# Optimization experiments

Measured on AMD Instinct MI355X. Metric: run time of the kernel, lower is better.

## Reference

```python
import jax, jax.numpy as jnp
import numpy as np
import math

B, S, E, H = 2, 1024, 1024, 8
HD = E // H
M, W, K, GH, R, MR = 128, 32, 8, 128, 8, 8
ATTN_ALPHA, GATE_TEMP, CONTENT_MIX = 3.0, 1.0, 0.25
FFN_H = 4 * E


def _layernorm(z, g, b):
    mu = jnp.mean(z, axis=-1, keepdims=True)
    var = jnp.var(z, axis=-1, keepdims=True)
    return (z - mu) * jax.lax.rsqrt(var + 1e-5) * g + b


def _topk_sparse(logits, k, temp):
    # faithful to torch topk_sparse_weights: hard + (soft - hard).detach()
    soft = jax.nn.softmax(logits / max(temp, 1e-6), axis=-1)
    idx = jax.lax.top_k(soft, k)[1]
    hard = jax.nn.one_hot(idx, logits.shape[-1], dtype=soft.dtype).sum(axis=-2)
    hard = hard / (hard.sum(axis=-1, keepdims=True) + 1e-8)
    return hard + jax.lax.stop_gradient(soft - hard)


def _pos_and_window():
    rel = jnp.arange(-(S - 1), S, dtype=jnp.float32)  # [2S-1]
    p1 = rel / S
    p2 = jnp.sign(rel) * jnp.sqrt(jnp.abs(rel) + 1e-6) / math.sqrt(S)
    pos_kern = jnp.stack([p1, p2], axis=-1)  # [2S-1, 2]
    d = jnp.arange(S, dtype=jnp.float32)
    sigma = S / 4.0
    win = jnp.exp(-(d ** 2) / (2.0 * sigma ** 2))  # [S]
    return pos_kern, win


def setup_inputs() -> dict:
    key = jax.random.key(0)
    ks = jax.random.split(key, 20)
    rn = lambda i, shape, s: jax.random.normal(ks[i], shape, dtype=jnp.float32) * s
    scale = 1.0 / math.sqrt(HD)
    return {
        'x': rn(0, (B, S, E), 1.0),
        'v_w': rn(1, (E, E), 0.02), 'v_b': jnp.zeros((E,), jnp.float32),
        'out_w': rn(2, (E, E), 0.02), 'out_b': jnp.zeros((E,), jnp.float32),
        'qmod_w': rn(3, (E, H), 0.02), 'qmod_b': jnp.zeros((H,), jnp.float32),
        'kmod_w': rn(4, (E, H), 0.02), 'kmod_b': jnp.zeros((H,), jnp.float32),
        'gate_w1': rn(5, (H, E, GH), 0.02), 'gate_b1': jnp.zeros((H, GH), jnp.float32),
        'gate_w2': rn(6, (H, GH, M), 0.02), 'gate_b2': jnp.zeros((H, M), jnp.float32),
        'mod_w1': rn(7, (H, E, GH), 0.02), 'mod_b1': jnp.zeros((H, GH), jnp.float32),
        'mod_w2': rn(8, (H, GH, MR), 0.02), 'mod_b2': jnp.zeros((H, MR), jnp.float32),
        'mod_basis': rn(9, (H, MR, M), 0.05),
        'freqs': rn(10, (H, M, W, 2), 1.5),
        'amps': rn(11, (H, M, W), 0.02) + 0.5,
        'phases': rn(12, (H, M, W), math.pi),
        'content_wq': rn(13, (H, HD, R), scale),
        'content_wk': rn(14, (H, HD, R), scale),
        'ffn_w1': rn(15, (E, FFN_H), 0.02), 'ffn_b1': jnp.zeros((FFN_H,), jnp.float32),
        'ffn_w2': rn(16, (FFN_H, E), 0.02), 'ffn_b2': jnp.zeros((E,), jnp.float32),
        'ln_attn_g': jnp.ones((E,), jnp.float32), 'ln_attn_b': jnp.zeros((E,), jnp.float32),
        'ln_ffn_g': jnp.ones((E,), jnp.float32), 'ln_ffn_b': jnp.zeros((E,), jnp.float32),
    }


def reference(x, v_w, v_b, out_w, out_b, qmod_w, qmod_b, kmod_w, kmod_b,
              gate_w1, gate_b1, gate_w2, gate_b2, mod_w1, mod_b1, mod_w2, mod_b2,
              mod_basis, freqs, amps, phases, content_wq, content_wk,
              ffn_w1, ffn_b1, ffn_w2, ffn_b2, ln_attn_g, ln_attn_b, ln_ffn_g, ln_ffn_b):
    pos_kern, win = _pos_and_window()
    # --- per-sequence gating over mask library (top-k sparse routing) ---
    pooled = x.mean(axis=1)  # [B,E]
    gh = jax.nn.relu(jnp.einsum('be,heg->bhg', pooled, gate_w1) + gate_b1)
    glog = jnp.einsum('bhg,hgm->bhm', gh, gate_w2) + gate_b2  # [B,H,M]
    wsel = _topk_sparse(glog, K, GATE_TEMP)
    mh = jax.nn.relu(jnp.einsum('be,heg->bhg', pooled, mod_w1) + mod_b1)
    mr = jnp.einsum('bhg,hgr->bhr', mh, mod_w2) + mod_b2  # [B,H,MR]
    mod = jnp.einsum('bhr,hrm->bhm', mr, mod_basis)
    wmod = wsel * (1.0 + mod)  # [B,H,M]
    # --- wave-interference synthesis of relative-position kernels ---
    dots = jnp.einsum('ld,hmwd->hmwl', pos_kern, freqs)  # [H,M,W,2S-1]
    waves = jnp.sin(2.0 * math.pi * dots + phases[..., None]) * amps[..., None]
    kernels = waves.sum(axis=2)  # [H,M,2S-1]
    kern = jnp.einsum('bhm,hml->bhl', wmod, kernels)  # [B,H,2S-1]
    # --- Toeplitz gather into causal score matrix ---
    i = jnp.arange(S)
    rel_idx = (i[None, :] - i[:, None]) + (S - 1)  # index of rel = j - i
    scores = kern[:, :, rel_idx]  # [B,H,S,S]
    dist = jnp.clip(i[:, None] - i[None, :], 0, S - 1)
    scores = scores * win[dist]
    qs = x @ qmod_w + qmod_b  # [B,S,H]
    km = x @ kmod_w + kmod_b
    logits = ATTN_ALPHA * scores + qs.transpose(0, 2, 1)[..., None] + km.transpose(0, 2, 1)[:, :, None, :]
    # --- low-rank content term ---
    xh = x.reshape(B, S, H, HD)
    qc = jnp.einsum('bshd,hdr->bhsr', xh, content_wq)
    kc = jnp.einsum('bshd,hdr->bhsr', xh, content_wk)
    logits = logits + CONTENT_MIX * jnp.einsum('bhsr,bhtr->bhst', qc, kc)
    causal = i[:, None] >= i[None, :]
    logits = jnp.where(causal, logits, -jnp.inf)
    attn = jax.nn.softmax(logits, axis=-1)
    v = (x @ v_w + v_b).reshape(B, S, H, HD)
    o = jnp.einsum('bhst,bthd->bshd', attn, v).reshape(B, S, E)
    o = o @ out_w + out_b
    y = _layernorm(x + o, ln_attn_g, ln_attn_b)
    f = jax.nn.gelu(y @ ffn_w1 + ffn_b1) @ ffn_w2 + ffn_b2
    return _layernorm(y + f, ln_ffn_g, ln_ffn_b)
```

## Files before the change

kernel.cpp:

```cpp
#include <hip/hip_runtime.h>
#include <math.h>
#include <stdint.h>

namespace {

constexpr int B_ = 2, S_ = 1024, E_ = 1024, H_ = 8, HD_ = 128;
constexpr int M_ = 128, W_ = 32, GH_ = 128, R_ = 8, MR_ = 8, FFNH_ = 4096;
constexpr int SCH = 32;
constexpr int SPC = S_ / SCH;

typedef __bf16 bf16;
typedef _Float16 f16;
typedef __attribute__((ext_vector_type(8))) __bf16 bf16x8;
typedef __attribute__((ext_vector_type(4))) __bf16 bf16x4;
typedef __attribute__((ext_vector_type(4))) _Float16 f16x4;
typedef __attribute__((ext_vector_type(4))) float f32x4;

__device__ inline float gelu_tanh(float u) {
  float u3 = u * u * u;
  return 0.5f * u * (1.f + tanhf(0.7978845608028654f * (u + 0.044715f * u3)));
}

__device__ __forceinline__ void gl_lds16(const void* g, void* l) {
  __builtin_amdgcn_global_load_lds((const __attribute__((address_space(1))) void*)g,
                                   (__attribute__((address_space(3))) void*)l, 16, 0, 0);
}

template <int NB>
__device__ __forceinline__ void gemm_body(
    const bf16* __restrict__ A, const bf16* __restrict__ BT,
    f16* __restrict__ P, int N, int K, int Kslice, size_t strideB, size_t mn,
    int lin, int gx, int gy, bf16* Asb, bf16* Bsb) {
  int t = threadIdx.x;
  int by = lin % gy;
  int rem = lin / gy;
  int bx = rem % gx;
  int z = rem / gx;
  int bb = z % NB;
  int k0 = (z / NB) * Kslice;
  const bf16* Bbase = BT + (size_t)bb * strideB;
  int row0 = by * 128, col0 = bx * 128;
  int lane = t & 63, wid = t >> 6;
  int wr = wid >> 1, wc = wid & 1;

  const bf16* AgP[4];
  const bf16* BgP[4];
  int ldo[4];
#pragma unroll
  for (int j = 0; j < 4; ++j) {
    int p = t + j * 256;
    int sub = p >> 9;
    int pp = p & 511;
    int rt = ((pp >> 6) << 4) | (pp & 15);
    int kb = (pp >> 4) & 3;
    AgP[j] = A + (size_t)(row0 + rt) * K + k0 + sub * 32 + kb * 8;
    BgP[j] = Bbase + (size_t)(col0 + rt) * K + k0 + sub * 32 + kb * 8;
    ldo[j] = sub * 4096 + pp * 8;
  }

  f32x4 acc[4][4];
#pragma unroll
  for (int m = 0; m < 4; ++m)
#pragma unroll
    for (int n = 0; n < 4; ++n) acc[m][n] = (f32x4){0.f, 0.f, 0.f, 0.f};

#pragma unroll
  for (int j = 0; j < 4; ++j) {
    gl_lds16(AgP[j], &Asb[ldo[j]]);
    gl_lds16(BgP[j], &Bsb[ldo[j]]);
  }

  const int nt = Kslice >> 6;
  for (int kt = 0; kt < nt; ++kt) {
    int cur = kt & 1;
    __syncthreads();
    if (kt + 1 < nt) {
      size_t go = (size_t)(kt + 1) * 64;
      int nb = cur ^ 1;
#pragma unroll
      for (int j = 0; j < 4; ++j) {
        gl_lds16(AgP[j] + go, &Asb[nb * 8192 + ldo[j]]);
        gl_lds16(BgP[j] + go, &Bsb[nb * 8192 + ldo[j]]);
      }
    }
#pragma unroll
    for (int kk = 0; kk < 2; ++kk) {
      bf16x8 af[4], bfr[4];
#pragma unroll
      for (int m = 0; m < 4; ++m)
        af[m] = *(const bf16x8*)&Asb[cur * 8192 + kk * 4096 + ((wr * 4 + m) * 64 + lane) * 8];
#pragma unroll
      for (int n = 0; n < 4; ++n)
        bfr[n] = *(const bf16x8*)&Bsb[cur * 8192 + kk * 4096 + ((wc * 4 + n) * 64 + lane) * 8];
#pragma unroll
      for (int m = 0; m < 4; ++m)
#pragma unroll
        for (int n = 0; n < 4; ++n)
          acc[m][n] = __builtin_amdgcn_mfma_f32_16x16x32_bf16(af[m], bfr[n], acc[m][n], 0, 0, 0);
    }
  }

  f16* Pz = P + (size_t)z * mn;
  int r0 = row0 + wr * 64, c0 = col0 + wc * 64;
#pragma unroll
  for (int m = 0; m < 4; ++m)
#pragma unroll
    for (int n = 0; n < 4; ++n) {
      int col = c0 + n * 16 + (lane & 15);
#pragma unroll
      for (int reg = 0; reg < 4; ++reg) {
        int row = r0 + m * 16 + ((lane >> 4) << 2) + reg;
        Pz[(size_t)row * N + col] = (f16)acc[m][n][reg];
      }
    }
}

__global__ __launch_bounds__(256) void k_prep(
    const float* __restrict__ x, bf16* __restrict__ xb,
    const float* __restrict__ v_w, bf16* __restrict__ vwT,
    const float* __restrict__ out_w, bf16* __restrict__ outwT,
    const float* __restrict__ ffn_w1, bf16* __restrict__ ffn1T,
    const float* __restrict__ ffn_w2, bf16* __restrict__ ffn2T,
    const float* __restrict__ qmw, const float* __restrict__ kmw,
    const float* __restrict__ cwq, const float* __restrict__ cwk,
    bf16* __restrict__ wcat, float* __restrict__ part,
    const float* __restrict__ freqs, const float* __restrict__ amps,
    const float* __restrict__ phases, float* __restrict__ kerns) {
  __shared__ float tile[32][33];
  __shared__ float f0[W_], f1[W_], am[W_], ph[W_];
  int b = blockIdx.x, t = threadIdx.x;
  if (b < 2048) {
    size_t i = ((size_t)b * 256 + t) * 4;
    float4 v = *(const float4*)(x + i);
    bf16x4 o;
    o.x = (bf16)v.x; o.y = (bf16)v.y; o.z = (bf16)v.z; o.w = (bf16)v.w;
    *(bf16x4*)(xb + i) = o;
    return;
  }
  if (b < 12288) {
    const float* w; bf16* wT; int K, N, bx, by;
    if (b < 3072) {
      w = v_w; wT = vwT; K = 1024; N = 1024;
      int l = b - 2048; bx = l & 31; by = l >> 5;
    } else if (b < 4096) {
      w = out_w; wT = outwT; K = 1024; N = 1024;
      int l = b - 3072; bx = l & 31; by = l >> 5;
    } else if (b < 8192) {
      w = ffn_w1; wT = ffn1T; K = 1024; N = 4096;
      int l = b - 4096; bx = l & 127; by = l >> 7;
    } else {
      w = ffn_w2; wT = ffn2T; K = 4096; N = 1024;
      int l = b - 8192; bx = l & 31; by = l >> 5;
    }
    int n0 = bx * 32, k0 = by * 32;
    int tx = t & 31, ty = t >> 5;
    for (int r = ty; r < 32; r += 8) tile[r][tx] = w[(size_t)(k0 + r) * N + n0 + tx];
    __syncthreads();
    for (int r = ty; r < 32; r += 8) wT[(size_t)(n0 + r) * K + k0 + tx] = (bf16)tile[tx][r];
    return;
  }
  if (b < 13312) {
    int idx = (b - 12288) * 256 + t;
    int n = idx >> 10, k = idx & 1023;
    float v = 0.f;
    if (n < 8) {
      v = qmw[k * 8 + n];
    } else if (n < 16) {
      v = kmw[k * 8 + (n - 8)];
    } else if (n < 80) {
      int u = n - 16, h = u >> 3, r = u & 7;
      int kk = k - h * 128;
      if (kk >= 0 && kk < 128) v = cwq[((size_t)h * 128 + kk) * 8 + r];
    } else if (n < 144) {
      int u = n - 80, h = u >> 3, r = u & 7;
      int kk = k - h * 128;
      if (kk >= 0 && kk < 128) v = cwk[((size_t)h * 128 + kk) * 8 + r];
    }
    wcat[idx] = (bf16)v;
    return;
  }
  if (b < 13376) {
    int b0 = b - 13312;
    int bb = b0 / SCH, c = b0 % SCH;
    const float* xp = x + (size_t)bb * S_ * E_ + (size_t)c * SPC * E_;
    float acc[4] = {0.f, 0.f, 0.f, 0.f};
    for (int s = 0; s < SPC; ++s) {
      const float* row = xp + (size_t)s * E_;
#pragma unroll
      for (int q = 0; q < 4; ++q) acc[q] += row[t + q * 256];
    }
    float* pp = part + (size_t)b0 * E_;
#pragma unroll
    for (int q = 0; q < 4; ++q) pp[t + q * 256] = acc[q];
    return;
  }
  {
    int blk = b - 13376;
    int lt = blk & 3;
    int hm = blk >> 2;
    if (t < W_) {
      f0[t] = freqs[((size_t)hm * W_ + t) * 2 + 0];
      f1[t] = freqs[((size_t)hm * W_ + t) * 2 + 1];
      am[t] = amps[(size_t)hm * W_ + t];
      ph[t] = phases[(size_t)hm * W_ + t];
    }
    __syncthreads();
    int l = lt * 256 + t;
    float rel = (float)(l - (S_ - 1));
    float p1 = rel * (1.0f / S_);
    float p2 = (rel < 0.f) ? (-sqrtf(-rel + 1e-6f) * (1.0f / 32.0f)) : 0.f;
    const float TWO_PI = 6.28318530717958647692f;
    float acc = 0.f;
#pragma unroll
    for (int w = 0; w < W_; ++w)
      acc += am[w] * __sinf(TWO_PI * (f0[w] * p1 + f1[w] * p2) + ph[w]);
    kerns[(size_t)hm * S_ + l] = acc;
  }
}

__global__ __launch_bounds__(256) void k_qkg(
    const bf16* __restrict__ xb, const bf16* __restrict__ wcatT,
    f16* __restrict__ P,
    const float* __restrict__ part,
    const float* __restrict__ gw1, const float* __restrict__ mw1,
    float2* __restrict__ gpart) {
  __shared__ bf16 Asb[2 * 8192];
  __shared__ bf16 Bsb[2 * 8192];
  __shared__ float spool[2][64];
  __shared__ float red[2][2][128];
  int b = blockIdx.x, t = threadIdx.x;
  if (b < 256) {
    int lin = (b & 7) * 32 + (b >> 3);
    gemm_body<1>(xb, wcatT, P, 256, E_, 128, 0, (size_t)2048 * 256,
                 lin, 2, 16, Asb, Bsb);
    return;
  }
  int b0 = b - 256;
  int chunk = b0 & 15, h = (b0 >> 4) & 7, mat = b0 >> 7;
  const float* w = mat ? mw1 : gw1;
  if (t < 128) {
    int bb = t >> 6;
    int e = chunk * 64 + (t & 63);
    float s = 0.f;
    for (int c = 0; c < SCH; ++c) s += part[(size_t)(bb * SCH + c) * E_ + e];
    spool[bb][t & 63] = s * (1.0f / S_);
  }
  __syncthreads();
  int g = t & 127, half = t >> 7;
  int e0 = chunk * 64 + half * 32;
  const float* wp = w + (size_t)h * E_ * GH_ + (size_t)e0 * GH_ + g;
  float a0 = 0.f, a1 = 0.f;
#pragma unroll 8
  for (int r = 0; r < 32; ++r) {
    float wv = wp[(size_t)r * GH_];
    a0 += spool[0][half * 32 + r] * wv;
    a1 += spool[1][half * 32 + r] * wv;
  }
  red[half][0][g] = a0;
  red[half][1][g] = a1;
  __syncthreads();
  if (half == 0) {
    float2 o;
    o.x = red[0][0][g] + red[1][0][g];
    o.y = red[0][1][g] + red[1][1][g];
    gpart[(((size_t)mat * H_ + h) * 16 + chunk) * 128 + g] = o;
  }
}

__global__ __launch_bounds__(256) void k_fg2(
    const f16* __restrict__ P, const float* __restrict__ qmb,
    const float* __restrict__ kmb, float* __restrict__ qsT,
    float* __restrict__ kmT, float* __restrict__ qc, float* __restrict__ kc,
    const float2* __restrict__ gpart,
    const float* __restrict__ gb1, const float* __restrict__ gw2, const float* __restrict__ gb2,
    const float* __restrict__ mb1, const float* __restrict__ mw2, const float* __restrict__ mb2,
    const float* __restrict__ mbasis, float* __restrict__ wmod) {
  __shared__ float ghs[GH_], mhs[GH_], glog[M_], mrs[MR_];
  __shared__ float red2[2][128];
  __shared__ float rbuf[128];
  int blk = blockIdx.x, t = threadIdx.x;
  if (blk < 2048) {
    if (t >= 144) return;
    int row = blk;
    int b = row >> 10, s = row & 1023;
    const size_t mn = (size_t)2048 * 256;
    float sum = 0.f;
#pragma unroll
    for (int z = 0; z < 8; ++z) sum += (float)P[(size_t)z * mn + (size_t)row * 256 + t];
    if (t < 8) {
      qsT[((size_t)(b * 8 + t)) * 1024 + s] = sum + qmb[t];
    } else if (t < 16) {
      kmT[((size_t)(b * 8 + t - 8)) * 1024 + s] = sum + kmb[t - 8];
    } else if (t < 80) {
      int u = t - 16, h = u >> 3, r = u & 7;
      qc[(((size_t)(b * 8 + h)) * 1024 + s) * 8 + r] = sum;
    } else {
      int u = t - 80, h = u >> 3, r = u & 7;
      kc[(((size_t)(b * 8 + h)) * 1024 + s) * 8 + r] = sum;
    }
    return;
  }
  int bh = blk - 2048;
  int b = bh >> 3, h = bh & 7;
  {
    int g = t & 127, mat = t >> 7;
    const float2* pp = gpart + ((size_t)mat * H_ + h) * 16 * 128 + g;
    float acc = 0.f;
#pragma unroll
    for (int c = 0; c < 16; ++c) {
      float2 v = pp[(size_t)c * 128];
      acc += b ? v.y : v.x;
    }
    acc += (mat ? mb1 : gb1)[h * GH_ + g];
    acc = fmaxf(acc, 0.f);
    if (mat == 0) ghs[g] = acc; else mhs[g] = acc;
  }
  __syncthreads();
  {
    int m = t & 127, half = t >> 7;
    float acc = 0.f;
    const float* wp = gw2 + (size_t)h * GH_ * M_ + m;
#pragma unroll 4
    for (int g = half * 64; g < half * 64 + 64; ++g)
      acc += ghs[g] * wp[(size_t)g * M_];
    red2[half][m] = acc;
  }
  __syncthreads();
  if (t < 128) glog[t] = red2[0][t] + red2[1][t] + gb2[h * M_ + t];
  if (t < 64) {
    int r = t & 7, seg = t >> 3;
    float acc = 0.f;
    const float* wp = mw2 + (size_t)h * GH_ * MR_ + r;
    for (int g = seg * 16; g < seg * 16 + 16; ++g) acc += mhs[g] * wp[(size_t)g * MR_];
    acc += __shfl_xor(acc, 8);
    acc += __shfl_xor(acc, 16);
    acc += __shfl_xor(acc, 32);
    if (t < 8) mrs[t] = acc + mb2[h * MR_ + t];
  }
  __syncthreads();
  if (t < 128) rbuf[t] = glog[t];
  __syncthreads();
  for (int off = 64; off >= 1; off >>= 1) {
    if (t < off) rbuf[t] = fmaxf(rbuf[t], rbuf[t + off]);
    __syncthreads();
  }
  float mx = rbuf[0];
  __syncthreads();
  float ev = 0.f;
  if (t < 128) ev = expf(glog[t] - mx);
  __syncthreads();
  if (t < 128) rbuf[t] = ev;
  __syncthreads();
  for (int off = 64; off >= 1; off >>= 1) {
    if (t < off) rbuf[t] += rbuf[t + off];
    __syncthreads();
  }
  float inv = 1.f / rbuf[0];
  if (t < 128) {
    float wsel = ev * inv;
    float md = 0.f;
#pragma unroll
    for (int r = 0; r < MR_; ++r) md += mrs[r] * mbasis[((size_t)h * MR_ + r) * M_ + t];
    wmod[bh * M_ + t] = wsel * (1.f + md);
  }
}

__global__ __launch_bounds__(256) void k_cv(
    const float* __restrict__ qc, const float* __restrict__ kc,
    bf16* __restrict__ cont,
    const float* __restrict__ wmod, const float* __restrict__ kerns,
    float* __restrict__ swin,
    const bf16* __restrict__ vwT, const bf16* __restrict__ xb,
    f16* __restrict__ P) {
  __shared__ bf16 Asb[2 * 8192];
  __shared__ bf16 Bsb[2 * 8192];
  __shared__ float wm[M_];
  int b = blockIdx.x, t = threadIdx.x;
  if (b >= 1088) {
    int l = b - 1088;
    int lin = (l & 7) * 64 + (l >> 3);
    gemm_body<2>(vwT, xb, P, S_, E_, 256, (size_t)S_ * E_, (size_t)1024 * 1024,
                 lin, 8, 8, Asb, Bsb);
    return;
  }
  int jt = b & 7, it = (b >> 3) & 7, bh = b >> 6;
  if (bh == 16) {
    int blk = it * 8 + jt;
    int dt = blk & 3;
    int sbh = blk >> 2;
    int h = sbh & 7;
    if (t < M_) wm[t] = wmod[sbh * M_ + t];
    __syncthreads();
    int d = dt * 256 + t;
    int l = (S_ - 1) - d;
    float acc = 0.f;
    for (int m = 0; m < M_; ++m) acc += wm[m] * kerns[((size_t)h * M_ + m) * S_ + l];
    float dd = (float)d;
    float win = expf(-dd * dd * (1.0f / 131072.0f));
    swin[(size_t)sbh * S_ + d] = 3.0f * win * acc;
    return;
  }
  if (jt > it) return;
  int w = t >> 6, lane = t & 63;
  int ln = lane & 15, ko = lane >> 4;
  int i0 = it * 128 + w * 32;
  int j0 = jt * 128;

  bf16x8 av[2];
#pragma unroll
  for (int mi = 0; mi < 2; ++mi) {
    bf16x8 a;
#pragma unroll
    for (int k = 0; k < 8; ++k) a[k] = (bf16)0.f;
    if (ko == 0) {
      const float* qp = &qc[((size_t)bh * S_ + i0 + mi * 16 + ln) * 8];
      float4 q0 = *(const float4*)qp;
      float4 q1 = *(const float4*)(qp + 4);
      a[0] = (bf16)q0.x; a[1] = (bf16)q0.y; a[2] = (bf16)q0.z; a[3] = (bf16)q0.w;
      a[4] = (bf16)q1.x; a[5] = (bf16)q1.y; a[6] = (bf16)q1.z; a[7] = (bf16)q1.w;
    }
    av[mi] = a;
  }
  bf16x8 bv[8];
#pragma unroll
  for (int nb = 0; nb < 8; ++nb) {
    bf16x8 bb;
#pragma unroll
    for (int k = 0; k < 8; ++k) bb[k] = (bf16)0.f;
    if (ko == 0) {
      const float* kp = &kc[((size_t)bh * S_ + j0 + nb * 16 + ln) * 8];
      float4 k0 = *(const float4*)kp;
      float4 k1 = *(const float4*)(kp + 4);
      bb[0] = (bf16)k0.x; bb[1] = (bf16)k0.y; bb[2] = (bf16)k0.z; bb[3] = (bf16)k0.w;
      bb[4] = (bf16)k1.x; bb[5] = (bf16)k1.y; bb[6] = (bf16)k1.z; bb[7] = (bf16)k1.w;
    }
    bv[nb] = bb;
  }
  f32x4 acc[2][8];
#pragma unroll
  for (int mi = 0; mi < 2; ++mi)
#pragma unroll
    for (int nb = 0; nb < 8; ++nb) {
      acc[mi][nb] = (f32x4){0.f, 0.f, 0.f, 0.f};
      acc[mi][nb] = __builtin_amdgcn_mfma_f32_16x16x32_bf16(av[mi], bv[nb], acc[mi][nb], 0, 0, 0);
    }
  bf16* cb = cont + ((size_t)bh << 20);
#pragma unroll
  for (int mi = 0; mi < 2; ++mi)
#pragma unroll
    for (int nb = 0; nb < 8; ++nb) {
      int col = j0 + nb * 16 + ln;
#pragma unroll
      for (int reg = 0; reg < 4; ++reg) {
        int row = i0 + mi * 16 + ko * 4 + reg;
        cb[(size_t)row * S_ + col] = (bf16)acc[mi][nb][reg];
      }
    }
}

template <bool GELU, bool RES, bool OUTF32, bool OUTBF16>
__global__ __launch_bounds__(256) void k_gemm_mfma(
    const bf16* __restrict__ A, const bf16* __restrict__ BT,
    const float* __restrict__ bias, const float* __restrict__ res,
    float* __restrict__ C, bf16* __restrict__ Cb, int N, int K) {
  __shared__ bf16 Asb[2][8192];
  __shared__ bf16 Bsb[2][8192];
  int t = threadIdx.x;
  int gx = gridDim.x, gy = gridDim.y;
  int nwg = gx * gy;
  int lin = blockIdx.y * gx + blockIdx.x;
  if (!(nwg & 7)) {
    int cpx = nwg >> 3;
    lin = (lin & 7) * cpx + (lin >> 3);
  }
  int by = lin % gy;
  int bx = lin / gy;
  int row0 = by * 128, col0 = bx * 128;
  int lane = t & 63, wid = t >> 6;
  int wr = wid >> 1, wc = wid & 1;

  const bf16* AgP[4];
  const bf16* BgP[4];
  int ldo[4];
#pragma unroll
  for (int j = 0; j < 4; ++j) {
    int p = t + j * 256;
    int sub = p >> 9;
    int pp = p & 511;
    int rt = ((pp >> 6) << 4) | (pp & 15);
    int kb = (pp >> 4) & 3;
    AgP[j] = A + (size_t)(row0 + rt) * K + sub * 32 + kb * 8;
    BgP[j] = BT + (size_t)(col0 + rt) * K + sub * 32 + kb * 8;
    ldo[j] = sub * 4096 + pp * 8;
  }

  f32x4 acc[4][4];
#pragma unroll
  for (int m = 0; m < 4; ++m)
#pragma unroll
    for (int n = 0; n < 4; ++n) acc[m][n] = (f32x4){0.f, 0.f, 0.f, 0.f};

#pragma unroll
  for (int j = 0; j < 4; ++j) {
    gl_lds16(AgP[j], &Asb[0][ldo[j]]);
    gl_lds16(BgP[j], &Bsb[0][ldo[j]]);
  }

  const int nt = K >> 6;
  for (int kt = 0; kt < nt; ++kt) {
    int cur = kt & 1;
    __syncthreads();
    if (kt + 1 < nt) {
      size_t go = (size_t)(kt + 1) * 64;
      int nb = cur ^ 1;
#pragma unroll
      for (int j = 0; j < 4; ++j) {
        gl_lds16(AgP[j] + go, &Asb[nb][ldo[j]]);
        gl_lds16(BgP[j] + go, &Bsb[nb][ldo[j]]);
      }
    }
#pragma unroll
    for (int kk = 0; kk < 2; ++kk) {
      bf16x8 af[4], bfr[4];
#pragma unroll
      for (int m = 0; m < 4; ++m)
        af[m] = *(const bf16x8*)&Asb[cur][kk * 4096 + ((wr * 4 + m) * 64 + lane) * 8];
#pragma unroll
      for (int n = 0; n < 4; ++n)
        bfr[n] = *(const bf16x8*)&Bsb[cur][kk * 4096 + ((wc * 4 + n) * 64 + lane) * 8];
#pragma unroll
      for (int m = 0; m < 4; ++m)
#pragma unroll
        for (int n = 0; n < 4; ++n)
          acc[m][n] = __builtin_amdgcn_mfma_f32_16x16x32_bf16(af[m], bfr[n], acc[m][n], 0, 0, 0);
    }
  }

  int r0 = row0 + wr * 64, c0 = col0 + wc * 64;
#pragma unroll
  for (int m = 0; m < 4; ++m) {
#pragma unroll
    for (int n = 0; n < 4; ++n) {
      int col = c0 + n * 16 + (lane & 15);
      float bcol = bias[col];
#pragma unroll
      for (int reg = 0; reg < 4; ++reg) {
        int row = r0 + m * 16 + ((lane >> 4) << 2) + reg;
        float u = acc[m][n][reg] + bcol;
        if (GELU) u = gelu_tanh(u);
        if (RES) u += res[(size_t)row * N + col];
        if (OUTF32) C[(size_t)row * N + col] = u;
        if (OUTBF16) Cb[(size_t)row * N + col] = (bf16)u;
      }
    }
  }
}

template <int NB>
__global__ __launch_bounds__(256) void k_gemm_sk(
    const bf16* __restrict__ A, const bf16* __restrict__ BT,
    f16* __restrict__ P, int N, int K, int Kslice, size_t strideB, size_t mn) {
  __shared__ bf16 Asb[2 * 8192];
  __shared__ bf16 Bsb[2 * 8192];
  int gx = gridDim.x, gy = gridDim.y;
  int nwg = gx * gy * gridDim.z;
  int lin = (blockIdx.z * gy + blockIdx.y) * gx + blockIdx.x;
  if (!(nwg & 7)) {
    int cpx = nwg >> 3;
    lin = (lin & 7) * cpx + (lin >> 3);
  }
  gemm_body<NB>(A, BT, P, N, K, Kslice, strideB, mn, lin, gx, gy, Asb, Bsb);
}

__global__ __launch_bounds__(256) void k_fin_vT(const f16* __restrict__ P,
                                                const float* __restrict__ bias,
                                                bf16* __restrict__ vT) {
  size_t i = ((size_t)blockIdx.x * 256 + threadIdx.x) * 4;
  const size_t mn = (size_t)1024 * 1024;
  float sx = 0.f, sy = 0.f, sz = 0.f, sw2 = 0.f;
#pragma unroll
  for (int sk = 0; sk < 4; ++sk) {
    f16x4 v = *(const f16x4*)&P[(size_t)sk * 2 * mn + i];
    sx += (float)v.x; sy += (float)v.y; sz += (float)v.z; sw2 += (float)v.w;
  }
  float bcol = bias[(i >> 10) & 1023];
  bf16x4 o;
  o.x = (bf16)(sx + bcol); o.y = (bf16)(sy + bcol);
  o.z = (bf16)(sz + bcol); o.w = (bf16)(sw2 + bcol);
  *(bf16x4*)&vT[i] = o;
}

template <int SK, bool OUTBF16>
__global__ __launch_bounds__(256) void k_fin_ln(
    const f16* __restrict__ P, const float* __restrict__ bias,
    const float* __restrict__ res, const float* __restrict__ g,
    const float* __restrict__ bb, float* __restrict__ outF,
    bf16* __restrict__ outB) {
  int row = blockIdx.x, t = threadIdx.x;
  size_t base = (size_t)row * E_ + t * 4;
  const size_t mn = (size_t)2048 * 1024;
  float u0 = 0.f, u1 = 0.f, u2 = 0.f, u3 = 0.f;
#pragma unroll
  for (int sk = 0; sk < SK; ++sk) {
    f16x4 v = *(const f16x4*)&P[(size_t)sk * mn + base];
    u0 += (float)v.x; u1 += (float)v.y; u2 += (float)v.z; u3 += (float)v.w;
  }
  float4 bv = *(const float4*)&bias[t * 4];
  float4 rv = *(const float4*)&res[base];
  u0 += bv.x + rv.x; u1 += bv.y + rv.y; u2 += bv.z + rv.z; u3 += bv.w + rv.w;
  float s = u0 + u1 + u2 + u3;
  float s2 = u0 * u0 + u1 * u1 + u2 * u2 + u3 * u3;
#pragma unroll
  for (int off = 32; off >= 1; off >>= 1) {
    s += __shfl_xor(s, off);
    s2 += __shfl_xor(s2, off);
  }
  __shared__ float rs[4], rs2[4];
  int wid = t >> 6;
  if ((t & 63) == 0) { rs[wid] = s; rs2[wid] = s2; }
  __syncthreads();
  float S1 = rs[0] + rs[1] + rs[2] + rs[3];
  float S2 = rs2[0] + rs2[1] + rs2[2] + rs2[3];
  float mu = S1 * (1.f / E_);
  float var = S2 * (1.f / E_) - mu * mu;
  float inv = rsqrtf(var + 1e-5f);
  float4 gv = *(const float4*)&g[t * 4];
  float4 bbv = *(const float4*)&bb[t * 4];
  float4 ov;
  ov.x = (u0 - mu) * inv * gv.x + bbv.x;
  ov.y = (u1 - mu) * inv * gv.y + bbv.y;
  ov.z = (u2 - mu) * inv * gv.z + bbv.z;
  ov.w = (u3 - mu) * inv * gv.w + bbv.w;
  *(float4*)&outF[base] = ov;
  if (OUTBF16) {
    bf16x4 obv;
    obv.x = (bf16)ov.x; obv.y = (bf16)ov.y; obv.z = (bf16)ov.z; obv.w = (bf16)ov.w;
    *(bf16x4*)&outB[base] = obv;
  }
}

__global__ __launch_bounds__(256) void k_attn2(
    const float* __restrict__ qsT, const float* __restrict__ kmT,
    const bf16* __restrict__ cont, const float* __restrict__ swin,
    const bf16* __restrict__ vT,
    bf16* __restrict__ o, bf16* __restrict__ opart, float* __restrict__ mlpart) {
  int q = blockIdx.x & 3;
  int iwg = blockIdx.x >> 2;
  if (q > iwg) return;
  int bh = blockIdx.y;
  int b = bh >> 3, h = bh & 7;
  int t = threadIdx.x;
  int wid = t >> 6, lane = t & 63;
  int iw = iwg * 4 + wid;
  int m = lane & 15, ko = lane >> 4;
  int ntile = iwg + 1;

  __shared__ float sw[S_];
  *(float4*)&sw[t * 4] = *(const float4*)&swin[(size_t)bh * S_ + t * 4];
  __syncthreads();

  int i_row = iw * 16 + m;
  float qs_i = qsT[(size_t)bh * S_ + i_row];
  const bf16* cr = cont + ((size_t)bh << 20) + (size_t)i_row * S_;

  f32x4 acc[8];
#pragma unroll
  for (int nf = 0; nf < 8; ++nf) acc[nf] = (f32x4){0.f, 0.f, 0.f, 0.f};
  float m_run = -INFINITY, l_run = 0.f;

  for (int jt = q; jt < ntile; jt += 4) {
    int j0 = jt * 64;
    float pv[2][8];
    float mx = -INFINITY;
    bf16x8 cv[2];
    cv[0] = *(const bf16x8*)&cr[j0 + ko * 8];
    cv[1] = *(const bf16x8*)&cr[j0 + 32 + ko * 8];
#pragma unroll
    for (int s = 0; s < 2; ++s) {
      int bj = j0 + s * 32 + ko * 8;
      float4 km0 = *(const float4*)&kmT[(size_t)bh * S_ + bj];
      float4 km1 = *(const float4*)&kmT[(size_t)bh * S_ + bj + 4];
      float kmv[8] = {km0.x, km0.y, km0.z, km0.w, km1.x, km1.y, km1.z, km1.w};
#pragma unroll
      for (int e = 0; e < 8; ++e) {
        int j = bj + e;
        int dd = i_row - j;
        float val = sw[dd >= 0 ? dd : 0] + qs_i + kmv[e] + 0.25f * (float)cv[s][e];
        val = (dd >= 0) ? val : -INFINITY;
        pv[s][e] = val;
        mx = fmaxf(mx, val);
      }
    }
    mx = fmaxf(mx, __shfl_xor(mx, 16));
    mx = fmaxf(mx, __shfl_xor(mx, 32));
    float mnew = fmaxf(m_run, mx);
    float scale = __expf(m_run - mnew);
    float lsum = 0.f;
    bf16x8 pa[2];
#pragma unroll
    for (int s = 0; s < 2; ++s)
#pragma unroll
      for (int e = 0; e < 8; ++e) {
        float p = __expf(pv[s][e] - mnew);
        lsum += p;
        pa[s][e] = (bf16)p;
      }
    lsum += __shfl_xor(lsum, 16);
    lsum += __shfl_xor(lsum, 32);
    l_run = l_run * scale + lsum;
    m_run = mnew;
    float sc[4];
#pragma unroll
    for (int r = 0; r < 4; ++r) sc[r] = __shfl(scale, ko * 4 + r);
#pragma unroll
    for (int nf = 0; nf < 8; ++nf)
#pragma unroll
      for (int r = 0; r < 4; ++r) acc[nf][r] *= sc[r];
#pragma unroll
    for (int s = 0; s < 2; ++s) {
      int bj = j0 + s * 32 + ko * 8;
#pragma unroll
      for (int nf = 0; nf < 8; ++nf) {
        int d = nf * 16 + m;
        bf16x8 bv = *(const bf16x8*)&vT[((size_t)bh * HD_ + d) * S_ + bj];
        acc[nf] = __builtin_amdgcn_mfma_f32_16x16x32_bf16(pa[s], bv, acc[nf], 0, 0, 0);
      }
    }
  }

  if (ntile == 1) {
    float lr[4];
#pragma unroll
    for (int r = 0; r < 4; ++r) lr[r] = __shfl(l_run, ko * 4 + r);
#pragma unroll
    for (int nf = 0; nf < 8; ++nf) {
      int d = nf * 16 + m;
#pragma unroll
      for (int r = 0; r < 4; ++r) {
        int row = iw * 16 + ko * 4 + r;
        o[(((size_t)b * S_ + row) * H_ + h) * HD_ + d] = (bf16)(acc[nf][r] / lr[r]);
      }
    }
  } else {
    bf16* op = opart + ((size_t)(q * 16 + bh) * 64 + iw) * 2048;
#pragma unroll
    for (int nf = 0; nf < 8; ++nf) {
      int d = nf * 16 + m;
#pragma unroll
      for (int r = 0; r < 4; ++r) op[(ko * 4 + r) * 128 + d] = (bf16)acc[nf][r];
    }
    if (lane < 16) {
      float* mlp = mlpart + ((size_t)(q * 16 + bh) * 64 + iw) * 32;
      mlp[m * 2 + 0] = m_run;
      mlp[m * 2 + 1] = l_run;
    }
  }
}

__global__ __launch_bounds__(256) void k_comb(const bf16* __restrict__ opart,
                                              const float* __restrict__ mlpart,
                                              bf16* __restrict__ o) {
  int blk = blockIdx.x;
  int bh = blk / 60, iw = blk % 60 + 4;
  int b = bh >> 3, h = bh & 7;
  int t = threadIdx.x;
  int r = t >> 4, d0 = (t & 15) * 8;
  int nq = iw / 4 + 1;
  if (nq > 4) nq = 4;
  float mq[4], lq[4];
  float mm = -INFINITY;
#pragma unroll
  for (int q = 0; q < 4; ++q) {
    if (q < nq) {
      size_t idx = (size_t)(q * 16 + bh) * 64 + iw;
      mq[q] = mlpart[idx * 32 + r * 2];
      lq[q] = mlpart[idx * 32 + r * 2 + 1];
      mm = fmaxf(mm, mq[q]);
    }
  }
  float L = 0.f;
  float acc[8] = {0.f, 0.f, 0.f, 0.f, 0.f, 0.f, 0.f, 0.f};
#pragma unroll
  for (int q = 0; q < 4; ++q) {
    if (q < nq) {
      float e = __expf(mq[q] - mm);
      L += lq[q] * e;
      size_t idx = (size_t)(q * 16 + bh) * 64 + iw;
      bf16x8 v = *(const bf16x8*)&opart[(idx * 16 + r) * 128 + d0];
#pragma unroll
      for (int k = 0; k < 8; ++k) acc[k] += (float)v[k] * e;
    }
  }
  float inv = 1.f / L;
  bf16x8 ov;
#pragma unroll
  for (int k = 0; k < 8; ++k) ov[k] = (bf16)(acc[k] * inv);
  int row = iw * 16 + r;
  *(bf16x8*)&o[(((size_t)b * S_ + row) * H_ + h) * HD_ + d0] = ov;
}

}

extern "C" void kernel_launch(void* const* d_in, const int* in_sizes, int n_in,
                              void* d_out, int out_size, void* d_ws, size_t ws_size,
                              hipStream_t stream) {
  (void)in_sizes; (void)n_in; (void)out_size; (void)ws_size;
  const float* x       = (const float*)d_in[0];
  const float* v_w     = (const float*)d_in[1];
  const float* v_b     = (const float*)d_in[2];
  const float* out_w   = (const float*)d_in[3];
  const float* out_b   = (const float*)d_in[4];
  const float* qmod_w  = (const float*)d_in[5];
  const float* qmod_b  = (const float*)d_in[6];
  const float* kmod_w  = (const float*)d_in[7];
  const float* kmod_b  = (const float*)d_in[8];
  const float* gate_w1 = (const float*)d_in[9];
  const float* gate_b1 = (const float*)d_in[10];
  const float* gate_w2 = (const float*)d_in[11];
  const float* gate_b2 = (const float*)d_in[12];
  const float* mod_w1  = (const float*)d_in[13];
  const float* mod_b1  = (const float*)d_in[14];
  const float* mod_w2  = (const float*)d_in[15];
  const float* mod_b2  = (const float*)d_in[16];
  const float* mod_basis = (const float*)d_in[17];
  const float* freqs   = (const float*)d_in[18];
  const float* amps    = (const float*)d_in[19];
  const float* phases  = (const float*)d_in[20];
  const float* cwq     = (const float*)d_in[21];
  const float* cwk     = (const float*)d_in[22];
  const float* ffn_w1  = (const float*)d_in[23];
  const float* ffn_b1  = (const float*)d_in[24];
  const float* ffn_w2  = (const float*)d_in[25];
  const float* ffn_b2  = (const float*)d_in[26];
  const float* ln_ag   = (const float*)d_in[27];
  const float* ln_ab   = (const float*)d_in[28];
  const float* ln_fg   = (const float*)d_in[29];
  const float* ln_fb   = (const float*)d_in[30];

  char* wsc = (char*)d_ws;
  size_t off = 0;
  auto alloc = [&](size_t bytes) -> void* {
    void* p = wsc + off;
    off += (bytes + 255) & ~(size_t)255;
    return p;
  };
  float* pooled = (float*)alloc(2048 * 4);
  float* part   = (float*)alloc(65536 * 4);
  float2* gpart = (float2*)alloc((size_t)2 * H_ * 16 * 128 * 8);
  float* wmod   = (float*)alloc(2048 * 4);
  float* kerns  = (float*)alloc((size_t)H_ * M_ * S_ * 4);
  float* swin   = (float*)alloc((size_t)B_ * H_ * S_ * 4);
  float* qsT    = (float*)alloc((size_t)B_ * H_ * S_ * 4);
  float* kmT    = (float*)alloc((size_t)B_ * H_ * S_ * 4);
  float* qcb    = (float*)alloc((size_t)B_ * H_ * S_ * R_ * 4);
  float* kcb    = (float*)alloc((size_t)B_ * H_ * S_ * R_ * 4);
  float* ybuf   = (float*)alloc((size_t)B_ * S_ * E_ * 4);
  bf16* xb      = (bf16*)alloc((size_t)B_ * S_ * E_ * 2);
  bf16* yb      = (bf16*)alloc((size_t)B_ * S_ * E_ * 2);
  bf16* vwT     = (bf16*)alloc((size_t)E_ * E_ * 2);
  bf16* outwT   = (bf16*)alloc((size_t)E_ * E_ * 2);
  bf16* ffn1T   = (bf16*)alloc((size_t)E_ * FFNH_ * 2);
  bf16* ffn2T   = (bf16*)alloc((size_t)FFNH_ * E_ * 2);
  bf16* wcatT   = (bf16*)alloc((size_t)256 * E_ * 2);
  bf16* vT      = (bf16*)alloc((size_t)B_ * S_ * E_ * 2);
  bf16* ob      = (bf16*)alloc((size_t)B_ * S_ * E_ * 2);
  float* mlpart = (float*)alloc((size_t)4 * 16 * 64 * 16 * 2 * 4);
  char* poolU2  = (char*)alloc((size_t)B_ * S_ * FFNH_ * 2);
  bf16* opart = (bf16*)poolU2;
  bf16* hb    = (bf16*)poolU2;
  char* P1c = (char*)alloc((size_t)64 * 1024 * 1024);
  f16*  P1  = (f16*)P1c;
  bf16* cont = (bf16*)(P1c + (size_t)16 * 1024 * 1024);
  (void)pooled;

  float* outp = (float*)d_out;
  const int BS = B_ * S_;

  k_prep<<<17472, 256, 0, stream>>>(x, xb, v_w, vwT, out_w, outwT,
                                    ffn_w1, ffn1T, ffn_w2, ffn2T,
                                    qmod_w, kmod_w, cwq, cwk, wcatT,
                                    part, freqs, amps, phases, kerns);

  k_qkg<<<512, 256, 0, stream>>>(xb, wcatT, P1, part, gate_w1, mod_w1, gpart);

  k_fg2<<<2064, 256, 0, stream>>>(P1, qmod_b, kmod_b, qsT, kmT, qcb, kcb,
                                  gpart, gate_b1, gate_w2, gate_b2,
                                  mod_b1, mod_w2, mod_b2, mod_basis, wmod);

  k_cv<<<1600, 256, 0, stream>>>(qcb, kcb, cont, wmod, kerns, swin,
                                 vwT, xb, P1);
  k_fin_vT<<<2048, 256, 0, stream>>>(P1, v_b, vT);

  k_attn2<<<dim3(64, 16), 256, 0, stream>>>(qsT, kmT, cont, swin, vT, ob, opart, mlpart);
  k_comb<<<16 * 60, 256, 0, stream>>>(opart, mlpart, ob);

  k_gemm_sk<1><<<dim3(8, 16, 4), 256, 0, stream>>>(
      ob, outwT, P1, E_, E_, 256, 0, (size_t)2048 * 1024);
  k_fin_ln<4, true><<<2048, 256, 0, stream>>>(P1, out_b, x, ln_ag, ln_ab, ybuf, yb);

  k_gemm_mfma<true, false, false, true><<<dim3(FFNH_ / 128, BS / 128), 256, 0, stream>>>(
      yb, ffn1T, ffn_b1, nullptr, nullptr, hb, FFNH_, E_);

  k_gemm_sk<1><<<dim3(8, 16, 4), 256, 0, stream>>>(
      hb, ffn2T, P1, E_, FFNH_, 1024, 0, (size_t)2048 * 1024);
  k_fin_ln<4, false><<<2048, 256, 0, stream>>>(P1, ffn_b2, ybuf, ln_fg, ln_fb, outp, nullptr);
}
```

Measured before the change: 228.2 us.

## Move V projection GEMM into QK/gate kernel and fuse V finalize

The split-K V projection GEMM moves out of the content-score kernel into the earlier QK/gate-pooling kernel, and its reduction into bf16 vT moves into the fg2 kernel. This removes the separate k_fin_vT launch and lets the V GEMM run alongside the small QK GEMM and gating work, with the content kernel left lighter. The V partials go to a separate region of the scratch buffer at offset 48MB so they do not collide with the QK partials or the content buffer. The cost is a rebalanced schedule where the heavy GEMM blocks now share a launch with very different block types.

```diff
diff --git a/kernel.cpp b/kernel.cpp
--- a/kernel.cpp
+++ b/kernel.cpp
@@ -218,9 +218,10 @@
   }
 }
 
-__global__ __launch_bounds__(256) void k_qkg(
+__global__ __launch_bounds__(256) void k_qv(
     const bf16* __restrict__ xb, const bf16* __restrict__ wcatT,
-    f16* __restrict__ P,
+    f16* __restrict__ Pqk, f16* __restrict__ Pv,
+    const bf16* __restrict__ vwT,
     const float* __restrict__ part,
     const float* __restrict__ gw1, const float* __restrict__ mw1,
     float2* __restrict__ gpart) {
@@ -231,8 +232,15 @@
   int b = blockIdx.x, t = threadIdx.x;
   if (b < 256) {
     int lin = (b & 7) * 32 + (b >> 3);
-    gemm_body<1>(xb, wcatT, P, 256, E_, 128, 0, (size_t)2048 * 256,
+    gemm_body<1>(xb, wcatT, Pqk, 256, E_, 128, 0, (size_t)2048 * 256,
                  lin, 2, 16, Asb, Bsb);
+    return;
+  }
+  if (b >= 512) {
+    int l = b - 512;
+    int lin = (l & 7) * 64 + (l >> 3);
+    gemm_body<2>(vwT, xb, Pv, S_, E_, 256, (size_t)S_ * E_, (size_t)1024 * 1024,
+                 lin, 8, 8, Asb, Bsb);
     return;
   }
   int b0 = b - 256;
@@ -267,14 +275,16 @@
   }
 }
 
-__global__ __launch_bounds__(256) void k_fg2(
-    const f16* __restrict__ P, const float* __restrict__ qmb,
+__global__ __launch_bounds__(256) void k_fg2v(
+    const f16* __restrict__ Pqk, const float* __restrict__ qmb,
     const float* __restrict__ kmb, float* __restrict__ qsT,
     float* __restrict__ kmT, float* __restrict__ qc, float* __restrict__ kc,
     const float2* __restrict__ gpart,
     const float* __restrict__ gb1, const float* __restrict__ gw2, const float* __restrict__ gb2,
     const float* __restrict__ mb1, const float* __restrict__ mw2, const float* __restrict__ mb2,
-    const float* __restrict__ mbasis, float* __restrict__ wmod) {
+    const float* __restrict__ mbasis, float* __restrict__ wmod,
+    const f16* __restrict__ Pv, const float* __restrict__ v_b,
+    bf16* __restrict__ vT) {
   __shared__ float ghs[GH_], mhs[GH_], glog[M_], mrs[MR_];
   __shared__ float red2[2][128];
   __shared__ float rbuf[128];
@@ -286,7 +296,7 @@
     const size_t mn = (size_t)2048 * 256;
     float sum = 0.f;
 #pragma unroll
-    for (int z = 0; z < 8; ++z) sum += (float)P[(size_t)z * mn + (size_t)row * 256 + t];
+    for (int z = 0; z < 8; ++z) sum += (float)Pqk[(size_t)z * mn + (size_t)row * 256 + t];
     if (t < 8) {
       qsT[((size_t)(b * 8 + t)) * 1024 + s] = sum + qmb[t];
     } else if (t < 16) {
@@ -300,6 +310,22 @@
     }
     return;
   }
+  if (blk >= 2064) {
+    size_t i = ((size_t)(blk - 2064) * 256 + t) * 4;
+    const size_t mn = (size_t)1024 * 1024;
+    float sx = 0.f, sy = 0.f, sz = 0.f, sw2 = 0.f;
+#pragma unroll
+    for (int sk = 0; sk < 4; ++sk) {
+      f16x4 v = *(const f16x4*)&Pv[(size_t)sk * 2 * mn + i];
+      sx += (float)v.x; sy += (float)v.y; sz += (float)v.z; sw2 += (float)v.w;
+    }
+    float bcol = v_b[(i >> 10) & 1023];
+    bf16x4 o;
+    o.x = (bf16)(sx + bcol); o.y = (bf16)(sy + bcol);
+    o.z = (bf16)(sz + bcol); o.w = (bf16)(sw2 + bcol);
+    *(bf16x4*)&vT[i] = o;
+    return;
+  }
   int bh = blk - 2048;
   int b = bh >> 3, h = bh & 7;
   {
@@ -365,24 +391,13 @@
   }
 }
 
-__global__ __launch_bounds__(256) void k_cv(
+__global__ __launch_bounds__(256) void k_cs(
     const float* __restrict__ qc, const float* __restrict__ kc,
     bf16* __restrict__ cont,
     const float* __restrict__ wmod, const float* __restrict__ kerns,
-    float* __restrict__ swin,
-    const bf16* __restrict__ vwT, const bf16* __restrict__ xb,
-    f16* __restrict__ P) {
-  __shared__ bf16 Asb[2 * 8192];
-  __shared__ bf16 Bsb[2 * 8192];
+    float* __restrict__ swin) {
   __shared__ float wm[M_];
   int b = blockIdx.x, t = threadIdx.x;
-  if (b >= 1088) {
-    int l = b - 1088;
-    int lin = (l & 7) * 64 + (l >> 3);
-    gemm_body<2>(vwT, xb, P, S_, E_, 256, (size_t)S_ * E_, (size_t)1024 * 1024,
-                 lin, 8, 8, Asb, Bsb);
-    return;
-  }
   int jt = b & 7, it = (b >> 3) & 7, bh = b >> 6;
   if (bh == 16) {
     int blk = it * 8 + jt;
@@ -570,24 +585,6 @@
     lin = (lin & 7) * cpx + (lin >> 3);
   }
   gemm_body<NB>(A, BT, P, N, K, Kslice, strideB, mn, lin, gx, gy, Asb, Bsb);
-}
-
-__global__ __launch_bounds__(256) void k_fin_vT(const f16* __restrict__ P,
-                                                const float* __restrict__ bias,
-                                                bf16* __restrict__ vT) {
-  size_t i = ((size_t)blockIdx.x * 256 + threadIdx.x) * 4;
-  const size_t mn = (size_t)1024 * 1024;
-  float sx = 0.f, sy = 0.f, sz = 0.f, sw2 = 0.f;
-#pragma unroll
-  for (int sk = 0; sk < 4; ++sk) {
-    f16x4 v = *(const f16x4*)&P[(size_t)sk * 2 * mn + i];
-    sx += (float)v.x; sy += (float)v.y; sz += (float)v.z; sw2 += (float)v.w;
-  }
-  float bcol = bias[(i >> 10) & 1023];
-  bf16x4 o;
-  o.x = (bf16)(sx + bcol); o.y = (bf16)(sy + bcol);
-  o.z = (bf16)(sz + bcol); o.w = (bf16)(sw2 + bcol);
-  *(bf16x4*)&vT[i] = o;
 }
 
 template <int SK, bool OUTBF16>
@@ -871,6 +868,7 @@
   char* P1c = (char*)alloc((size_t)64 * 1024 * 1024);
   f16*  P1  = (f16*)P1c;
   bf16* cont = (bf16*)(P1c + (size_t)16 * 1024 * 1024);
+  f16*  P1v  = (f16*)(P1c + (size_t)48 * 1024 * 1024);
   (void)pooled;
 
   float* outp = (float*)d_out;
@@ -881,15 +879,15 @@
                                     qmod_w, kmod_w, cwq, cwk, wcatT,
                                     part, freqs, amps, phases, kerns);
 
-  k_qkg<<<512, 256, 0, stream>>>(xb, wcatT, P1, part, gate_w1, mod_w1, gpart);
-
-  k_fg2<<<2064, 256, 0, stream>>>(P1, qmod_b, kmod_b, qsT, kmT, qcb, kcb,
-                                  gpart, gate_b1, gate_w2, gate_b2,
-                                  mod_b1, mod_w2, mod_b2, mod_basis, wmod);
-
-  k_cv<<<1600, 256, 0, stream>>>(qcb, kcb, cont, wmod, kerns, swin,
-                                 vwT, xb, P1);
-  k_fin_vT<<<2048, 256, 0, stream>>>(P1, v_b, vT);
+  k_qv<<<1024, 256, 0, stream>>>(xb, wcatT, P1, P1v, vwT,
+                                 part, gate_w1, mod_w1, gpart);
+
+  k_fg2v<<<4112, 256, 0, stream>>>(P1, qmod_b, kmod_b, qsT, kmT, qcb, kcb,
+                                   gpart, gate_b1, gate_w2, gate_b2,
+                                   mod_b1, mod_w2, mod_b2, mod_basis, wmod,
+                                   P1v, v_b, vT);
+
+  k_cs<<<1088, 256, 0, stream>>>(qcb, kcb, cont, wmod, kerns, swin);
 
   k_attn2<<<dim3(64, 16), 256, 0, stream>>>(qsT, kmT, cont, swin, vT, ob, opart, mlpart);
   k_comb<<<16 * 60, 256, 0, stream>>>(opart, mlpart, ob);
```

Result: faster. 223.0 us (-2.3%).
